# Optimization experiments

Measured on AMD Instinct MI355X. Metric: run time of the kernel, lower is better.

## Reference

```python
import jax, jax.numpy as jnp
import numpy as np
from functools import partial

DN = ('NCHW', 'OIHW', 'NCHW')

def conv2d(x, w, b, stride):
    y = jax.lax.conv_general_dilated(x, w, (stride, stride), 'VALID', dimension_numbers=DN)
    return y + b[None, :, None, None]

def squash(s, eps=1e-8):
    norm = jnp.linalg.norm(s, axis=-1, keepdims=True)
    return (norm ** 2 / (1 + norm ** 2)) * s / (norm + eps)

def setup_inputs() -> dict:
    key = jax.random.key(0)
    ks = jax.random.split(key, 10)
    B, H, W = 16, 32, 512
    F, CAPS, E, OD = 64, 8, 8, 16
    H1 = (H - 6) // 2 + 1          # 14
    W1 = (W - 6) // 2 + 1          # 254
    N = F * H1 * W1 // CAPS        # 28448
    s = 0.05
    return {
        'x': jax.random.normal(ks[0], (B, H, W), jnp.float32),
        'conv1_w': jax.random.normal(ks[1], (F, 1, 6, 6), jnp.float32) * s,
        'conv1_b': jnp.zeros((F,), jnp.float32),
        'conv2_w': jax.random.normal(ks[2], (F, F, 6, 6), jnp.float32) * s,
        'conv2_b': jnp.zeros((F,), jnp.float32),
        'conv3_w': jax.random.normal(ks[3], (F, 2 * F, 1, 1), jnp.float32) * s,
        'conv3_b': jnp.zeros((F,), jnp.float32),
        'pc_w': jax.random.normal(ks[4], (N, CAPS, CAPS), jnp.float32) * s,  # [N, in, out]
        'pc_b': jnp.zeros((N, CAPS), jnp.float32),
        'ec_w': jax.random.normal(ks[5], (N, E, OD, CAPS), jnp.float32),
    }

def reference(x, conv1_w, conv1_b, conv2_w, conv2_b, conv3_w, conv3_b, pc_w, pc_b, ec_w):
    CAPS = pc_w.shape[1]
    NUM_ITER = 3
    B = x.shape[0]
    h = x[:, None]                                  # [B,1,H,W]
    h = jax.nn.relu(conv2d(h, conv1_w, conv1_b, 2)) # [B,F,14,254]
    y = jnp.pad(h, ((0, 0), (0, 0), (2, 3), (2, 3)))  # ZeroPad2d((2,3,2,3))
    y = jax.nn.relu(conv2d(y, conv2_w, conv2_b, 1))
    h = jax.nn.relu(jnp.concatenate((h, y), axis=1))
    h = conv2d(h, conv3_w, conv3_b, 1)              # [B,F,14,254]
    u_in = h.reshape(B, -1, CAPS)                   # [B,N,caps_len]
    # PrimaryCaps: N independent Linear(caps,caps) -> one batched einsum
    u = jnp.einsum('bni,nio->bno', u_in, pc_w) + pc_b[None]
    # EmotionCaps: per-capsule prediction u_hat [B,N,E,out_dim]
    u_hat = jnp.einsum('neoi,bni->bneo', ec_w, u)
    N, E = ec_w.shape[0], ec_w.shape[1]
    b_log = jnp.zeros((B, N, E), u_hat.dtype)
    v = None
    for r in range(NUM_ITER):
        c = jax.nn.softmax(b_log, axis=2)           # [B,N,E]
        s = jnp.einsum('bne,bneo->beo', c, u_hat)   # [B,E,out_dim]
        v = squash(s)
        if r < NUM_ITER - 1:
            b_log = b_log + jnp.einsum('bneo,beo->bne', u_hat, v)
    return jnp.linalg.norm(v, axis=-1)              # [B,E]
```

## Files before the change

### kernel.cpp

```cpp
#include <hip/hip_runtime.h>
#include <hip/hip_bf16.h>
#include <math.h>

#define BB 16
#define H1 14
#define W1 254
#define HPH 19
#define HPW2 264
#define NCAP 28448
#define FLATSZ 227584

typedef __attribute__((ext_vector_type(8))) short bf16x8;
typedef __attribute__((ext_vector_type(4))) float f32x4;

__device__ __forceinline__ ushort f2bf(float f) {
  __hip_bfloat16 h = __float2bfloat16(f);
  return *(ushort*)&h;
}

__global__ __launch_bounds__(256) void prep_w(const float* __restrict__ w2, const float* __restrict__ w3,
                                              ushort* __restrict__ wb, float* __restrict__ w3t) {
  int idx = blockIdx.x * 256 + threadIdx.x;
  if (idx < 147456) {
    int co = idx / 2304; int rem = idx - co * 2304;
    int tap = rem >> 6; int ci = rem & 63;
    wb[idx] = f2bf(w2[(co * 64 + ci) * 36 + tap]);
  }
  if (idx < 8192) {
    int co = idx & 63; int c = idx >> 6;
    w3t[idx] = w3[co * 128 + c];
  }
}

__global__ __launch_bounds__(256) void conv1_k(const float* __restrict__ x, const float* __restrict__ w1,
                                               const float* __restrict__ b1, float* __restrict__ hc) {
  const int i = blockIdx.x, b = blockIdx.y;
  __shared__ float xs[6 * 512];
  __shared__ float wsh[2304];
  __shared__ float bsh[64];
  const int t = threadIdx.x;
  for (int idx = t; idx < 6 * 512; idx += 256) {
    int r = idx >> 9, c = idx & 511;
    xs[idx] = x[((size_t)b * 32 + 2 * i + r) * 512 + c];
  }
  for (int idx = t; idx < 2304; idx += 256) wsh[idx] = w1[idx];
  if (t < 64) bsh[t] = b1[t];
  __syncthreads();
  if (t < 254) {
    for (int c = 0; c < 64; c++) {
      float acc = bsh[c];
#pragma unroll
      for (int p = 0; p < 6; p++)
#pragma unroll
        for (int q = 0; q < 6; q++)
          acc = fmaf(xs[p * 512 + 2 * t + q], wsh[c * 36 + p * 6 + q], acc);
      acc = fmaxf(acc, 0.f);
      hc[(((size_t)b * 64 + c) * H1 + i) * W1 + t] = acc;
    }
  }
}

__global__ __launch_bounds__(256) void nhwc_k(const float* __restrict__ hc, ushort* __restrict__ hpc) {
  const int ct = blockIdx.x, i = blockIdx.y, b = blockIdx.z;
  const int c0 = ct * 64;
  __shared__ float ls[64 * 65];
  const int t = threadIdx.x;
  for (int idx = t; idx < 4096; idx += 256) {
    int ci = idx >> 6, cc = idx & 63;
    int c = c0 + cc;
    ls[ci * 65 + cc] = (c < W1) ? hc[(((size_t)b * 64 + ci) * H1 + i) * W1 + c] : 0.f;
  }
  __syncthreads();
  uint* outp = (uint*)hpc;
  for (int idx = t; idx < 2048; idx += 256) {
    int cc = idx >> 5, ci2 = idx & 31;
    int c = c0 + cc;
    if (c < W1) {
      float f0 = ls[(2 * ci2) * 65 + cc];
      float f1 = ls[(2 * ci2 + 1) * 65 + cc];
      uint pk = (uint)f2bf(f0) | ((uint)f2bf(f1) << 16);
      outp[(((size_t)b * HPH + 2 + i) * HPW2 + 2 + c) * 32 + ci2] = pk;
    }
  }
}

__device__ __forceinline__ void stage_b(const ushort* __restrict__ wb, ushort* __restrict__ bbuf,
                                        int tap, int w, int l) {
#pragma unroll
  for (int r = 0; r < 2; r++) {
    int v = r * 256 + w * 64 + l;
    int co = v >> 3, s = v & 7;
    int g = s ^ (co & 7);
    const ushort* gp = wb + co * 2304 + tap * 64 + g * 8;
    ushort* lp = bbuf + (size_t)(r * 256 + w * 64) * 8;
    __builtin_amdgcn_global_load_lds((const uint*)gp, (uint*)lp, 16, 0, 0);
  }
}

__global__ __launch_bounds__(256, 1) void conv2_mfma(const ushort* __restrict__ hpc,
                                                     const ushort* __restrict__ wb,
                                                     const float* __restrict__ b2, float* __restrict__ y) {
  const int b = blockIdx.z, i = blockIdx.y, j0 = blockIdx.x * 128;
  const int t = threadIdx.x;
  const int w = t >> 6, l = t & 63;
  const int lr = l & 15, quad = l >> 4;

  __shared__ ushort bls[2][4096];

  f32x4 acc[2][4];
#pragma unroll
  for (int mt = 0; mt < 2; mt++)
#pragma unroll
    for (int nt = 0; nt < 4; nt++) acc[mt][nt] = (f32x4){0.f, 0.f, 0.f, 0.f};

  const ushort* abase = hpc + (((size_t)b * HPH + i) * HPW2 + (j0 + w * 32 + lr)) * 64 + quad * 8;

  bf16x8 a0[2][2], a1[2][2];

#define ALOAD(dst, tap)                                                        \
  {                                                                            \
    const int p_ = (tap) / 6, q_ = (tap) % 6;                                  \
    const ushort* ap_ = abase + ((size_t)p_ * HPW2 + q_) * 64;                 \
    dst[0][0] = *(const bf16x8*)(ap_);                                         \
    dst[0][1] = *(const bf16x8*)(ap_ + 1024);                                  \
    dst[1][0] = *(const bf16x8*)(ap_ + 32);                                    \
    dst[1][1] = *(const bf16x8*)(ap_ + 32 + 1024);                             \
  }

#define COMPUTE(a, bp)                                                         \
  {                                                                            \
    _Pragma("unroll")                                                          \
    for (int ch = 0; ch < 2; ch++) {                                           \
      const int g2 = ch * 4 + quad;                                            \
      _Pragma("unroll")                                                        \
      for (int nt = 0; nt < 4; nt++) {                                         \
        const int co = nt * 16 + lr;                                           \
        bf16x8 bf = *(const bf16x8*)((bp) + co * 64 + ((g2 ^ (co & 7)) * 8));  \
        acc[0][nt] = __builtin_amdgcn_mfma_f32_16x16x32_bf16(a[ch][0], bf, acc[0][nt], 0, 0, 0); \
        acc[1][nt] = __builtin_amdgcn_mfma_f32_16x16x32_bf16(a[ch][1], bf, acc[1][nt], 0, 0, 0); \
      }                                                                        \
    }                                                                          \
  }

  stage_b(wb, &bls[0][0], 0, w, l);
  __syncthreads();
  ALOAD(a0, 0);

  for (int tp = 0; tp < 36; tp += 2) {
    stage_b(wb, &bls[1][0], tp + 1, w, l);
    ALOAD(a1, tp + 1);
    COMPUTE(a0, &bls[0][0]);
    __syncthreads();
    if (tp + 2 < 36) {
      stage_b(wb, &bls[0][0], tp + 2, w, l);
      ALOAD(a0, tp + 2);
    }
    COMPUTE(a1, &bls[1][0]);
    __syncthreads();
  }

#pragma unroll
  for (int nt = 0; nt < 4; nt++) {
    const int co = nt * 16 + lr;
    const float bias = b2[co];
    float* yrow = y + (((size_t)b * 64 + co) * H1 + i) * W1;
#pragma unroll
    for (int mt = 0; mt < 2; mt++) {
      const int jb = j0 + w * 32 + mt * 16 + quad * 4;
#pragma unroll
      for (int r = 0; r < 4; r++) {
        int j = jb + r;
        if (j < W1) yrow[j] = fmaxf(acc[mt][nt][r] + bias, 0.f);
      }
    }
  }
#undef ALOAD
#undef COMPUTE
}

__global__ __launch_bounds__(256) void conv3_k(const float* __restrict__ hc, const float* __restrict__ y,
                                               const float* __restrict__ w3t, const float* __restrict__ b3,
                                               float* __restrict__ out3) {
  const int b = blockIdx.z, i = blockIdx.y, j0 = blockIdx.x * 64;
  __shared__ float cs[32][64];
  __shared__ float wsh[32][64];
  const int t = threadIdx.x;
  const int cog = t >> 4, jg = t & 15;
  float acc[4][4];
#pragma unroll
  for (int a = 0; a < 4; a++)
#pragma unroll
    for (int j = 0; j < 4; j++) acc[a][j] = 0.f;

  for (int ch = 0; ch < 4; ch++) {
    __syncthreads();
    for (int idx = t; idx < 2048; idx += 256) {
      int cl = idx >> 6; int j = j0 + (idx & 63);
      int c = ch * 32 + cl;
      float v = 0.f;
      if (j < W1) {
        if (c < 64) v = hc[(((size_t)b * 64 + c) * H1 + i) * W1 + j];
        else        v = y[(((size_t)b * 64 + (c - 64)) * H1 + i) * W1 + j];
      }
      cs[cl][idx & 63] = v;
    }
    for (int idx = t; idx < 2048; idx += 256)
      wsh[idx >> 6][idx & 63] = w3t[(ch * 32 + (idx >> 6)) * 64 + (idx & 63)];
    __syncthreads();
#pragma unroll
    for (int c = 0; c < 32; c++) {
      float4 xv = *(const float4*)&cs[c][jg * 4];
      float4 wv = *(const float4*)&wsh[c][cog * 4];
#pragma unroll
      for (int jj = 0; jj < 4; jj++) {
        float xx = (&xv.x)[jj];
        acc[0][jj] = fmaf(wv.x, xx, acc[0][jj]);
        acc[1][jj] = fmaf(wv.y, xx, acc[1][jj]);
        acc[2][jj] = fmaf(wv.z, xx, acc[2][jj]);
        acc[3][jj] = fmaf(wv.w, xx, acc[3][jj]);
      }
    }
  }
#pragma unroll
  for (int a = 0; a < 4; a++) {
    int co = cog * 4 + a;
    float bias = b3[co];
#pragma unroll
    for (int jj = 0; jj < 4; jj++) {
      int j = j0 + jg * 4 + jj;
      if (j < W1) out3[(((size_t)b * 64 + co) * H1 + i) * W1 + j] = acc[a][jj] + bias;
    }
  }
}

__global__ __launch_bounds__(256) void pc_k(const float* __restrict__ out3, const float* __restrict__ pcw,
                                            const float* __restrict__ pcb, float* __restrict__ u) {
  int n = blockIdx.x * 256 + threadIdx.x;
  if (n >= NCAP) return;
  float pw[64];
  const float4* pwp = (const float4*)(pcw + (size_t)n * 64);
#pragma unroll
  for (int k = 0; k < 16; k++) {
    float4 v = pwp[k];
    pw[4 * k] = v.x; pw[4 * k + 1] = v.y; pw[4 * k + 2] = v.z; pw[4 * k + 3] = v.w;
  }
  float pb[8];
  {
    const float4* pbp = (const float4*)(pcb + (size_t)n * 8);
    float4 a = pbp[0], b = pbp[1];
    pb[0] = a.x; pb[1] = a.y; pb[2] = a.z; pb[3] = a.w;
    pb[4] = b.x; pb[5] = b.y; pb[6] = b.z; pb[7] = b.w;
  }
  for (int b = 0; b < BB; b++) {
    const float4* uip = (const float4*)(out3 + (size_t)b * FLATSZ + (size_t)n * 8);
    float4 a = uip[0], c = uip[1];
    float ui[8] = {a.x, a.y, a.z, a.w, c.x, c.y, c.z, c.w};
    float uo[8];
#pragma unroll
    for (int o = 0; o < 8; o++) uo[o] = pb[o];
#pragma unroll
    for (int i2 = 0; i2 < 8; i2++)
#pragma unroll
      for (int o = 0; o < 8; o++) uo[o] = fmaf(ui[i2], pw[i2 * 8 + o], uo[o]);
    float4* up = (float4*)(u + ((size_t)b * NCAP + n) * 8);
    up[0] = make_float4(uo[0], uo[1], uo[2], uo[3]);
    up[1] = make_float4(uo[4], uo[5], uo[6], uo[7]);
  }
}

template <int MODE>
__global__ __launch_bounds__(256, 4) void route_k(const float* __restrict__ u, const float* __restrict__ ecw,
                                                  const float* __restrict__ v, float* __restrict__ sout) {
  const int t = threadIdx.x, l = t & 63, wv = t >> 6;
  const int b0 = blockIdx.y * 8;
  const int n0 = blockIdx.x * 32 + wv * 8;

  __shared__ float us[4][512];
  __shared__ float red[4096];
  __shared__ float vlds[1024];

  if (MODE) {
    for (int idx = t; idx < 1024; idx += 256) vlds[idx] = v[b0 * 128 + idx];
    __syncthreads();
  }

#pragma unroll
  for (int bb = 0; bb < 8; bb++)
    us[wv][bb * 64 + l] = u[((size_t)(b0 + bb) * NCAP + n0) * 8 + l];

  float sacc[16];
#pragma unroll
  for (int k = 0; k < 16; k++) sacc[k] = 0.f;

  for (int nn = 0; nn < 8; nn++) {
    const int n = n0 + nn;
    const float4* ep = (const float4*)(ecw + (size_t)n * 1024 + l * 16);
    float4 e0 = ep[0], e1 = ep[1], e2 = ep[2], e3 = ep[3];
    float ec[16] = {e0.x, e0.y, e0.z, e0.w, e1.x, e1.y, e1.z, e1.w,
                    e2.x, e2.y, e2.z, e2.w, e3.x, e3.y, e3.z, e3.w};
#pragma unroll
    for (int bb = 0; bb < 8; bb++) {
      const float4* up = (const float4*)&us[wv][bb * 64 + nn * 8];
      float4 ua = up[0], ubv = up[1];
      float uv[8] = {ua.x, ua.y, ua.z, ua.w, ubv.x, ubv.y, ubv.z, ubv.w};
      float h0 = 0.f, h1 = 0.f;
#pragma unroll
      for (int k = 0; k < 8; k++) { h0 = fmaf(ec[k], uv[k], h0); h1 = fmaf(ec[8 + k], uv[k], h1); }
      if (MODE == 0) {
        sacc[2 * bb] += h0; sacc[2 * bb + 1] += h1;
      } else {
        float2 vv = *(const float2*)&vlds[bb * 128 + 2 * l];
        float p = h0 * vv.x + h1 * vv.y;
        p += __shfl_xor(p, 1); p += __shfl_xor(p, 2); p += __shfl_xor(p, 4);
        float m = p;
        m = fmaxf(m, __shfl_xor(m, 8)); m = fmaxf(m, __shfl_xor(m, 16)); m = fmaxf(m, __shfl_xor(m, 32));
        float ex = __expf(p - m);
        float den = ex;
        den += __shfl_xor(den, 8); den += __shfl_xor(den, 16); den += __shfl_xor(den, 32);
        float cc = ex * __builtin_amdgcn_rcpf(den);
        sacc[2 * bb] = fmaf(cc, h0, sacc[2 * bb]);
        sacc[2 * bb + 1] = fmaf(cc, h1, sacc[2 * bb + 1]);
      }
    }
  }

#pragma unroll
  for (int k = 0; k < 16; k++) red[k * 256 + wv * 64 + l] = sacc[k];
  __syncthreads();
#pragma unroll
  for (int m = 0; m < 4; m++) {
    int slot = t + 256 * m;
    int bl = slot >> 7, eo = slot & 127;
    int k = 2 * bl + (eo & 1), l2 = eo >> 1;
    const float* r = red + k * 256 + l2;
    atomicAdd(&sout[(b0 + bl) * 128 + eo], r[0] + r[64] + r[128] + r[192]);
  }
}

__global__ void squash_k(const float* __restrict__ s, float scale, const float* __restrict__ vprev,
                         float* __restrict__ vout) {
  int t = threadIdx.x;
  const float* sp = s + t * 16;
  float sv[16]; float nn = 0.f;
#pragma unroll
  for (int o = 0; o < 16; o++) { float x = sp[o] * scale; sv[o] = x; nn = fmaf(x, x, nn); }
  float norm = sqrtf(nn);
  float f = nn / (1.f + nn) / (norm + 1e-8f);
#pragma unroll
  for (int o = 0; o < 16; o++) {
    float base = vprev ? vprev[t * 16 + o] : 0.f;
    vout[t * 16 + o] = base + f * sv[o];
  }
}

__global__ void squash_out_k(const float* __restrict__ s, float* __restrict__ out) {
  int t = threadIdx.x;
  float nn = 0.f;
#pragma unroll
  for (int o = 0; o < 16; o++) { float x = s[t * 16 + o]; nn = fmaf(x, x, nn); }
  float norm = sqrtf(nn);
  float f = nn / (1.f + nn) / (norm + 1e-8f);
  out[t] = f * norm;
}

extern "C" void kernel_launch(void* const* d_in, const int* in_sizes, int n_in,
                              void* d_out, int out_size, void* d_ws, size_t ws_size,
                              hipStream_t stream) {
  const float* x   = (const float*)d_in[0];
  const float* w1  = (const float*)d_in[1];
  const float* b1  = (const float*)d_in[2];
  const float* w2  = (const float*)d_in[3];
  const float* b2  = (const float*)d_in[4];
  const float* w3  = (const float*)d_in[5];
  const float* b3  = (const float*)d_in[6];
  const float* pcw = (const float*)d_in[7];
  const float* pcb = (const float*)d_in[8];
  const float* ecw = (const float*)d_in[9];
  float* out = (float*)d_out;

  float* ws = (float*)d_ws;
  size_t o = 0;
  float* hc   = ws + o; o += 3641344;
  float* yb   = ws + o; o += 3641344;
  float* out3 = ws + o; o += 3641344;
  ushort* hpc = (ushort*)(ws + o); o += 2568192;
  ushort* wb  = (ushort*)(ws + o); o += 73728;
  float* w3t  = ws + o; o += 8192;
  float* s0   = ws + o; o += 2048;
  float* s1   = ws + o; o += 2048;
  float* s2   = ws + o; o += 2048;
  float* v0   = ws + o; o += 2048;
  float* v1   = ws + o; o += 2048;
  float* ub   = hc;

  hipMemsetAsync(hpc, 0, (size_t)16 * HPH * HPW2 * 64 * 2, stream);
  hipMemsetAsync(s0, 0, 3 * 2048 * 4, stream);

  prep_w<<<576, 256, 0, stream>>>(w2, w3, wb, w3t);
  conv1_k<<<dim3(14, 16), 256, 0, stream>>>(x, w1, b1, hc);
  nhwc_k<<<dim3(4, 14, 16), 256, 0, stream>>>(hc, hpc);
  conv2_mfma<<<dim3(2, 14, 16), 256, 0, stream>>>(hpc, wb, b2, yb);
  conv3_k<<<dim3(4, 14, 16), 256, 0, stream>>>(hc, yb, w3t, b3, out3);
  pc_k<<<112, 256, 0, stream>>>(out3, pcw, pcb, ub);
  route_k<0><<<dim3(889, 2), 256, 0, stream>>>(ub, ecw, nullptr, s0);
  squash_k<<<1, 128, 0, stream>>>(s0, 0.125f, nullptr, v0);
  route_k<1><<<dim3(889, 2), 256, 0, stream>>>(ub, ecw, v0, s1);
  squash_k<<<1, 128, 0, stream>>>(s1, 1.0f, v0, v1);
  route_k<1><<<dim3(889, 2), 256, 0, stream>>>(ub, ecw, v1, s2);
  squash_out_k<<<1, 128, 0, stream>>>(s2, out);
}
```

Measured before the change: 495.4 us.

## Fuse routing iterations into one cooperative kernel with grid sync

Replaces the three routing launches and their separate squash kernels with one cooperative kernel. It uses grid.sync between passes and computes the squash inside the kernel. Each block now covers all 16 batches, so the large ecw tensor is streamed once per pass instead of once per batch half, and the next capsule's weights are prefetched. The softmax over the 8 emotions is done with DPP and swizzle lane reductions, using the accumulated v sum in place of an explicit b_log. A fallback to the old launch sequence covers a failed cooperative launch. The risks are the occupancy limit that cooperative residency imposes and atomics contention on the small s buffers.

```diff
diff --git a/kernel.cpp b/kernel.cpp
--- a/kernel.cpp
+++ b/kernel.cpp
@@ -1,6 +1,9 @@
 #include <hip/hip_runtime.h>
 #include <hip/hip_bf16.h>
+#include <hip/hip_cooperative_groups.h>
 #include <math.h>
+
+namespace cg = cooperative_groups;
 
 #define BB 16
 #define H1 14
@@ -265,6 +268,145 @@
     float4* up = (float4*)(u + ((size_t)b * NCAP + n) * 8);
     up[0] = make_float4(uo[0], uo[1], uo[2], uo[3]);
     up[1] = make_float4(uo[4], uo[5], uo[6], uo[7]);
+  }
+}
+
+template <int CTRL>
+__device__ __forceinline__ float dpp_add(float x) {
+  int y = __builtin_amdgcn_update_dpp(0, __float_as_int(x), CTRL, 0xF, 0xF, true);
+  return x + __int_as_float(y);
+}
+
+template <int R>
+__device__ __forceinline__ void route_pass(const float* __restrict__ u, const float* __restrict__ ecw,
+                                           float* __restrict__ sbuf, const float* vA, const float* vB,
+                                           float* red, const int n0, const int l, const int t,
+                                           const int xaddr) {
+  float sacc[32];
+#pragma unroll
+  for (int k = 0; k < 32; k++) sacc[k] = 0.f;
+
+  float4 c0, c1, c2, c3;
+  {
+    const float4* ep = (const float4*)(ecw + (size_t)n0 * 1024) + (l << 2);
+    c0 = ep[0]; c1 = ep[1]; c2 = ep[2]; c3 = ep[3];
+  }
+
+#pragma unroll 1
+  for (int nn = 0; nn < 8; nn++) {
+    const int n = n0 + nn;
+    const float ec[16] = {c0.x, c0.y, c0.z, c0.w, c1.x, c1.y, c1.z, c1.w,
+                          c2.x, c2.y, c2.z, c2.w, c3.x, c3.y, c3.z, c3.w};
+    if (nn < 7) {
+      const float4* ep = (const float4*)(ecw + (size_t)(n + 1) * 1024) + (l << 2);
+      c0 = ep[0]; c1 = ep[1]; c2 = ep[2]; c3 = ep[3];
+    }
+#pragma unroll
+    for (int bb = 0; bb < 16; bb++) {
+      const int off = __builtin_amdgcn_readfirstlane((bb * NCAP + n) * 8);
+      const float4 ua = *(const float4*)(u + off);
+      const float4 ub = *(const float4*)(u + off + 4);
+      const float uv[8] = {ua.x, ua.y, ua.z, ua.w, ub.x, ub.y, ub.z, ub.w};
+      float h0 = 0.f, h1 = 0.f;
+#pragma unroll
+      for (int k = 0; k < 8; k++) {
+        h0 = fmaf(ec[k], uv[k], h0);
+        h1 = fmaf(ec[8 + k], uv[k], h1);
+      }
+      if (R == 0) {
+        sacc[2 * bb] += h0;
+        sacc[2 * bb + 1] += h1;
+      } else {
+        float p = fmaf(h0, vA[bb * 64 + l], h1 * vB[bb * 64 + l]);
+        p = dpp_add<0xB1>(p);
+        p = dpp_add<0x4E>(p);
+        p = dpp_add<0x141>(p);
+        const float ex = __expf(p);
+        float den = dpp_add<0x140>(ex);
+        den += __int_as_float(__builtin_amdgcn_ds_swizzle(__float_as_int(den), 0x401F));
+        den += __int_as_float(__builtin_amdgcn_ds_bpermute(xaddr, __float_as_int(den)));
+        const float cc = ex * __builtin_amdgcn_rcpf(den);
+        sacc[2 * bb] = fmaf(cc, h0, sacc[2 * bb]);
+        sacc[2 * bb + 1] = fmaf(cc, h1, sacc[2 * bb + 1]);
+      }
+    }
+  }
+
+  __syncthreads();
+#pragma unroll
+  for (int k = 0; k < 32; k++) red[k * 256 + t] = sacc[k];
+  __syncthreads();
+#pragma unroll
+  for (int m = 0; m < 8; m++) {
+    const int S = t + 256 * m;
+    const int b = S >> 7, rem = S & 127, e = rem >> 4, o = rem & 15;
+    const float* rp = red + (2 * b + (o & 1)) * 256 + e * 8 + (o >> 1);
+    atomicAdd(&sbuf[S], rp[0] + rp[64] + rp[128] + rp[192]);
+  }
+}
+
+__global__ __launch_bounds__(256, 4) void route_fused(const float* __restrict__ u,
+                                                      const float* __restrict__ ecw,
+                                                      float* __restrict__ sb,
+                                                      float* __restrict__ out) {
+  __shared__ float red[8192];
+  __shared__ float vA[1024];
+  __shared__ float vB[1024];
+  const int t = threadIdx.x, l = t & 63;
+  const int wv = __builtin_amdgcn_readfirstlane(t >> 6);
+  const int n0 = blockIdx.x * 32 + wv * 8;
+  const int xaddr = (l ^ 32) << 2;
+  cg::grid_group grid = cg::this_grid();
+
+  route_pass<0>(u, ecw, sb, vA, vB, red, n0, l, t, xaddr);
+  grid.sync();
+  if (t < 128) {
+    float sv[16]; float q = 0.f;
+#pragma unroll
+    for (int o = 0; o < 16; o++) {
+      float x = 0.125f * __hip_atomic_load(&sb[t * 16 + o], __ATOMIC_RELAXED, __HIP_MEMORY_SCOPE_AGENT);
+      sv[o] = x; q = fmaf(x, x, q);
+    }
+    const float norm = sqrtf(q);
+    const float f = q / (1.f + q) / (norm + 1e-8f);
+#pragma unroll
+    for (int o = 0; o < 16; o++) {
+      const float vv = f * sv[o];
+      if (o & 1) vB[t * 8 + (o >> 1)] = vv; else vA[t * 8 + (o >> 1)] = vv;
+    }
+  }
+  __syncthreads();
+
+  route_pass<1>(u, ecw, sb + 2048, vA, vB, red, n0, l, t, xaddr);
+  grid.sync();
+  if (t < 128) {
+    float sv[16]; float q = 0.f;
+#pragma unroll
+    for (int o = 0; o < 16; o++) {
+      float x = __hip_atomic_load(&sb[2048 + t * 16 + o], __ATOMIC_RELAXED, __HIP_MEMORY_SCOPE_AGENT);
+      sv[o] = x; q = fmaf(x, x, q);
+    }
+    const float norm = sqrtf(q);
+    const float f = q / (1.f + q) / (norm + 1e-8f);
+#pragma unroll
+    for (int o = 0; o < 16; o++) {
+      const float vv = f * sv[o];
+      if (o & 1) vB[t * 8 + (o >> 1)] += vv; else vA[t * 8 + (o >> 1)] += vv;
+    }
+  }
+  __syncthreads();
+
+  route_pass<1>(u, ecw, sb + 4096, vA, vB, red, n0, l, t, xaddr);
+  grid.sync();
+  if (blockIdx.x == 0 && t < 128) {
+    float q = 0.f;
+#pragma unroll
+    for (int o = 0; o < 16; o++) {
+      float x = __hip_atomic_load(&sb[4096 + t * 16 + o], __ATOMIC_RELAXED, __HIP_MEMORY_SCOPE_AGENT);
+      q = fmaf(x, x, q);
+    }
+    const float norm = sqrtf(q);
+    out[t] = q / (1.f + q) * norm / (norm + 1e-8f);
   }
 }
 
@@ -402,10 +544,19 @@
   conv2_mfma<<<dim3(2, 14, 16), 256, 0, stream>>>(hpc, wb, b2, yb);
   conv3_k<<<dim3(4, 14, 16), 256, 0, stream>>>(hc, yb, w3t, b3, out3);
   pc_k<<<112, 256, 0, stream>>>(out3, pcw, pcb, ub);
-  route_k<0><<<dim3(889, 2), 256, 0, stream>>>(ub, ecw, nullptr, s0);
-  squash_k<<<1, 128, 0, stream>>>(s0, 0.125f, nullptr, v0);
-  route_k<1><<<dim3(889, 2), 256, 0, stream>>>(ub, ecw, v0, s1);
-  squash_k<<<1, 128, 0, stream>>>(s1, 1.0f, v0, v1);
-  route_k<1><<<dim3(889, 2), 256, 0, stream>>>(ub, ecw, v1, s2);
-  squash_out_k<<<1, 128, 0, stream>>>(s2, out);
-}
+
+  {
+    const float* uarg = ub;
+    void* args[] = {(void*)&uarg, (void*)&ecw, (void*)&s0, (void*)&out};
+    hipError_t ce = hipLaunchCooperativeKernel((void*)route_fused, dim3(889), dim3(256),
+                                               args, 0, stream);
+    if (ce != hipSuccess) {
+      route_k<0><<<dim3(889, 2), 256, 0, stream>>>(ub, ecw, nullptr, s0);
+      squash_k<<<1, 128, 0, stream>>>(s0, 0.125f, nullptr, v0);
+      route_k<1><<<dim3(889, 2), 256, 0, stream>>>(ub, ecw, v0, s1);
+      squash_k<<<1, 128, 0, stream>>>(s1, 1.0f, v0, v1);
+      route_k<1><<<dim3(889, 2), 256, 0, stream>>>(ub, ecw, v1, s2);
+      squash_out_k<<<1, 128, 0, stream>>>(s2, out);
+    }
+  }
+}
```

Result: slower. 783.1 us (+58.1%).

## Process all batches per routing block to halve ec_w traffic, DPP softmax reductions

Applied to the files above, without the earlier changes.

The routing kernel now has each block cover all 16 batch entries instead of 8. The large per-capsule ec_w weights are therefore streamed from memory once per routing pass instead of twice. It also double-buffers the ec_w loads across capsules and replaces the shuffle-based reductions with DPP, swizzle and bpermute. The softmax drops its max subtraction, which saves work but could overflow if the routing logits grow large. Each thread now holds twice as many accumulators, which raises register and LDS pressure under the 4-blocks-per-CU launch bound.

```diff
diff --git a/kernel.cpp b/kernel.cpp
--- a/kernel.cpp
+++ b/kernel.cpp
@@ -268,72 +268,93 @@
   }
 }
 
+template <int CTRL>
+__device__ __forceinline__ float dpp_add(float x) {
+  int y = __builtin_amdgcn_update_dpp(0, __float_as_int(x), CTRL, 0xF, 0xF, true);
+  return x + __int_as_float(y);
+}
+
 template <int MODE>
-__global__ __launch_bounds__(256, 4) void route_k(const float* __restrict__ u, const float* __restrict__ ecw,
-                                                  const float* __restrict__ v, float* __restrict__ sout) {
+__global__ __launch_bounds__(256, 4) void route2_k(const float* __restrict__ u, const float* __restrict__ ecw,
+                                                   const float* __restrict__ v, float* __restrict__ sout) {
+  __shared__ float red[8192];
+  __shared__ float vlds[2048];
+  float* us = red;
+
   const int t = threadIdx.x, l = t & 63, wv = t >> 6;
-  const int b0 = blockIdx.y * 8;
   const int n0 = blockIdx.x * 32 + wv * 8;
-
-  __shared__ float us[4][512];
-  __shared__ float red[4096];
-  __shared__ float vlds[1024];
+  const int xaddr = (l ^ 32) << 2;
 
   if (MODE) {
-    for (int idx = t; idx < 1024; idx += 256) vlds[idx] = v[b0 * 128 + idx];
-    __syncthreads();
-  }
-
-#pragma unroll
-  for (int bb = 0; bb < 8; bb++)
-    us[wv][bb * 64 + l] = u[((size_t)(b0 + bb) * NCAP + n0) * 8 + l];
-
-  float sacc[16];
-#pragma unroll
-  for (int k = 0; k < 16; k++) sacc[k] = 0.f;
-
-  for (int nn = 0; nn < 8; nn++) {
-    const int n = n0 + nn;
-    const float4* ep = (const float4*)(ecw + (size_t)n * 1024 + l * 16);
-    float4 e0 = ep[0], e1 = ep[1], e2 = ep[2], e3 = ep[3];
-    float ec[16] = {e0.x, e0.y, e0.z, e0.w, e1.x, e1.y, e1.z, e1.w,
-                    e2.x, e2.y, e2.z, e2.w, e3.x, e3.y, e3.z, e3.w};
-#pragma unroll
-    for (int bb = 0; bb < 8; bb++) {
-      const float4* up = (const float4*)&us[wv][bb * 64 + nn * 8];
-      float4 ua = up[0], ubv = up[1];
-      float uv[8] = {ua.x, ua.y, ua.z, ua.w, ubv.x, ubv.y, ubv.z, ubv.w};
+    for (int idx = t; idx < 2048; idx += 256) vlds[idx] = v[idx];
+  }
+#pragma unroll
+  for (int bb = 0; bb < 16; bb++)
+    us[wv * 1024 + bb * 64 + l] = u[((size_t)bb * NCAP + n0) * 8 + l];
+  if (MODE) __syncthreads();
+
+  float sacc[32];
+#pragma unroll
+  for (int k = 0; k < 32; k++) sacc[k] = 0.f;
+
+  const float4* ebase = (const float4*)(ecw + (size_t)n0 * 1024) + (l << 2);
+
+  auto proc = [&](int nn, float4 e0, float4 e1, float4 e2, float4 e3) {
+    const float ec[16] = {e0.x, e0.y, e0.z, e0.w, e1.x, e1.y, e1.z, e1.w,
+                          e2.x, e2.y, e2.z, e2.w, e3.x, e3.y, e3.z, e3.w};
+#pragma unroll
+    for (int bb = 0; bb < 16; bb++) {
+      const float4* up = (const float4*)&us[wv * 1024 + bb * 64 + nn * 8];
+      const float4 ua = up[0], ub = up[1];
+      const float uv[8] = {ua.x, ua.y, ua.z, ua.w, ub.x, ub.y, ub.z, ub.w};
       float h0 = 0.f, h1 = 0.f;
 #pragma unroll
-      for (int k = 0; k < 8; k++) { h0 = fmaf(ec[k], uv[k], h0); h1 = fmaf(ec[8 + k], uv[k], h1); }
+      for (int k = 0; k < 8; k++) {
+        h0 = fmaf(ec[k], uv[k], h0);
+        h1 = fmaf(ec[8 + k], uv[k], h1);
+      }
       if (MODE == 0) {
-        sacc[2 * bb] += h0; sacc[2 * bb + 1] += h1;
+        sacc[2 * bb] += h0;
+        sacc[2 * bb + 1] += h1;
       } else {
-        float2 vv = *(const float2*)&vlds[bb * 128 + 2 * l];
-        float p = h0 * vv.x + h1 * vv.y;
-        p += __shfl_xor(p, 1); p += __shfl_xor(p, 2); p += __shfl_xor(p, 4);
-        float m = p;
-        m = fmaxf(m, __shfl_xor(m, 8)); m = fmaxf(m, __shfl_xor(m, 16)); m = fmaxf(m, __shfl_xor(m, 32));
-        float ex = __expf(p - m);
-        float den = ex;
-        den += __shfl_xor(den, 8); den += __shfl_xor(den, 16); den += __shfl_xor(den, 32);
-        float cc = ex * __builtin_amdgcn_rcpf(den);
+        const float2 vv = *(const float2*)&vlds[bb * 128 + 2 * l];
+        float p = fmaf(h0, vv.x, h1 * vv.y);
+        p = dpp_add<0xB1>(p);
+        p = dpp_add<0x4E>(p);
+        p = dpp_add<0x141>(p);
+        const float ex = __expf(p);
+        float den = dpp_add<0x140>(ex);
+        den += __int_as_float(__builtin_amdgcn_ds_swizzle(__float_as_int(den), 0x401F));
+        den += __int_as_float(__builtin_amdgcn_ds_bpermute(xaddr, __float_as_int(den)));
+        const float cc = ex * __builtin_amdgcn_rcpf(den);
         sacc[2 * bb] = fmaf(cc, h0, sacc[2 * bb]);
         sacc[2 * bb + 1] = fmaf(cc, h1, sacc[2 * bb + 1]);
       }
     }
-  }
-
-#pragma unroll
-  for (int k = 0; k < 16; k++) red[k * 256 + wv * 64 + l] = sacc[k];
+  };
+
+  float4 ca0 = ebase[0], ca1 = ebase[1], ca2 = ebase[2], ca3 = ebase[3];
+  for (int nn = 0; nn < 8; nn += 2) {
+    const float4* pb = ebase + (nn + 1) * 64;
+    float4 cb0 = pb[0], cb1 = pb[1], cb2 = pb[2], cb3 = pb[3];
+    proc(nn, ca0, ca1, ca2, ca3);
+    if (nn + 2 < 8) {
+      const float4* pa = ebase + (nn + 2) * 64;
+      ca0 = pa[0]; ca1 = pa[1]; ca2 = pa[2]; ca3 = pa[3];
+    }
+    proc(nn + 1, cb0, cb1, cb2, cb3);
+  }
+
   __syncthreads();
 #pragma unroll
-  for (int m = 0; m < 4; m++) {
-    int slot = t + 256 * m;
-    int bl = slot >> 7, eo = slot & 127;
-    int k = 2 * bl + (eo & 1), l2 = eo >> 1;
-    const float* r = red + k * 256 + l2;
-    atomicAdd(&sout[(b0 + bl) * 128 + eo], r[0] + r[64] + r[128] + r[192]);
+  for (int k = 0; k < 32; k++) red[k * 256 + t] = sacc[k];
+  __syncthreads();
+#pragma unroll
+  for (int m = 0; m < 8; m++) {
+    const int S = t + 256 * m;
+    const int b = S >> 7, rem = S & 127, e = rem >> 4, o2 = rem & 15;
+    const float* rp = red + (2 * b + (o2 & 1)) * 256 + e * 8 + (o2 >> 1);
+    atomicAdd(&sout[S], rp[0] + rp[64] + rp[128] + rp[192]);
   }
 }
 
@@ -402,10 +423,11 @@
   conv2_mfma<<<dim3(2, 14, 16), 256, 0, stream>>>(hpc, wb, b2, yb);
   conv3_k<<<dim3(4, 14, 16), 256, 0, stream>>>(hc, yb, w3t, b3, out3);
   pc_k<<<112, 256, 0, stream>>>(out3, pcw, pcb, ub);
-  route_k<0><<<dim3(889, 2), 256, 0, stream>>>(ub, ecw, nullptr, s0);
+
+  route2_k<0><<<889, 256, 0, stream>>>(ub, ecw, nullptr, s0);
   squash_k<<<1, 128, 0, stream>>>(s0, 0.125f, nullptr, v0);
-  route_k<1><<<dim3(889, 2), 256, 0, stream>>>(ub, ecw, v0, s1);
+  route2_k<1><<<889, 256, 0, stream>>>(ub, ecw, v0, s1);
   squash_k<<<1, 128, 0, stream>>>(s1, 1.0f, v0, v1);
-  route_k<1><<<dim3(889, 2), 256, 0, stream>>>(ub, ecw, v1, s2);
+  route2_k<1><<<889, 256, 0, stream>>>(ub, ecw, v1, s2);
   squash_out_k<<<1, 128, 0, stream>>>(s2, out);
 }
```

New measurement: 521.2 us. 1.05x slower.
